# Optimization experiments

Hardware: AMD Instinct MI355X
Metric: run time of the kernel (lower is better)

## Reference

```python
import jax, jax.numpy as jnp
import numpy as np

N_NODES = 4096
N_EDGES = 32768
PE_DIM = 16
HIDDEN = 128


def setup_inputs() -> dict:
    key = jax.random.key(0)
    k_nodes, k_send, k_recv, k_w = jax.random.split(key, 4)
    nodes = jax.random.normal(k_nodes, (N_NODES, 8), dtype=jnp.float32)
    senders = jax.random.randint(k_send, (N_EDGES,), 0, N_NODES)
    receivers = jax.random.randint(k_recv, (N_EDGES,), 0, N_NODES)
    W = jax.random.normal(k_w, (PE_DIM, HIDDEN), dtype=jnp.float32) / np.sqrt(PE_DIM).astype(np.float32)
    b = jnp.zeros((HIDDEN,), dtype=jnp.float32)
    return {"nodes": nodes, "senders": senders, "receivers": receivers, "W": W, "b": b}


def reference(nodes, senders, receivers, W, b):
    n = nodes.shape[0]
    pe_dim = W.shape[0]
    # out-degree per node (clamped at 1, as in the original)
    ones = jnp.ones(senders.shape[0], dtype=jnp.float32)
    degree = jnp.maximum(jax.ops.segment_sum(ones, senders, num_segments=n), 1.0)
    inv_deg_e = (1.0 / degree)[senders]  # [E], per-edge 1/deg(sender)

    prob = jnp.eye(n, dtype=jnp.float32)  # [n, n] landing probabilities
    diags = []
    for _ in range(pe_dim):
        # gather sender rows, normalize, scatter-add into receiver rows
        msg = prob[senders] * inv_deg_e[:, None]           # [E, n]
        prob = jax.ops.segment_sum(msg, receivers, num_segments=n)  # [n, n]
        diags.append(jnp.diagonal(prob))                    # return probability A^k_ii
    pe = jnp.stack(diags, axis=-1)  # [n, pe_dim]
    return pe @ W + b               # [n, hidden]
```

## Files before the change

### kernel.cpp

```cpp
#include <hip/hip_runtime.h>

#define NN 4096
#define NE 32768
#define PED 16
#define HID 128
#define CW 16
#define NCHUNK 64
#define THREADS 1024
#define PASSES 4

typedef _Float16 h_t;
typedef _Float16 h8 __attribute__((ext_vector_type(8)));
typedef unsigned long long u64;

__device__ __forceinline__ int xp(int p) {
  int g = ((p & 3) << 1) | ((p >> 2) & 1);
  return ((p >> 2) << 7) | (g << 4);
}


__global__ void count_kernel(const int* __restrict__ senders,
                             const int* __restrict__ receivers,
                             int* __restrict__ outdeg, int* __restrict__ indeg) {
  int e = blockIdx.x * blockDim.x + threadIdx.x;
  if (e < NE) {
    atomicAdd(&outdeg[senders[e]], 1);
    atomicAdd(&indeg[receivers[e]], 1);
  }
}

__global__ void perm_kernel(const int* __restrict__ outdeg, int* __restrict__ indeg,
                            float* __restrict__ dinv, int* __restrict__ fillc,
                            int* __restrict__ rowperm, int* __restrict__ sortpos,
                            int* __restrict__ chunk_off, int* __restrict__ chunk_len) {
  __shared__ int ld_d[NN];
  __shared__ int hist[64];
  __shared__ int hbase[64];
  int t = threadIdx.x;
  if (t < 64) hist[t] = 0;
  __syncthreads();
  for (int r = t; r < NN; r += 1024) {
    int od = outdeg[r]; if (od < 1) od = 1;
    dinv[r] = 1.0f / (float)od;
    fillc[r] = 0;
    int d = indeg[r]; if (d > 63) d = 63;
    ld_d[r] = d;
    indeg[r] = d;
    atomicAdd(&hist[d], 1);
  }
  __syncthreads();
  if (t == 0) {
    int acc = 0;
    for (int i = 0; i < 64; ++i) { hbase[i] = acc; acc += hist[i]; }
  }
  __syncthreads();
  for (int r = t; r < NN; r += 1024) {
    int pos = atomicAdd(&hbase[ld_d[r]], 1);
    rowperm[pos] = r;
    sortpos[r] = pos;
  }
  __syncthreads();
  if (t < NCHUNK) {
    int m = 0;
    for (int i = 0; i < 64; ++i) {
      int d = ld_d[rowperm[(t << 6) + i]];
      if (d > m) m = d;
    }
    chunk_len[t] = (m + 1) & ~1;
  }
  __syncthreads();
  if (t == 0) {
    int acc = 0;
    for (int c = 0; c < NCHUNK; ++c) { chunk_off[c] = acc; acc += chunk_len[c] << 6; }
    chunk_off[NCHUNK] = acc;
  }
}

__global__ void fill_ell(const int* __restrict__ senders, const int* __restrict__ receivers,
                         const int* __restrict__ sortpos, const int* __restrict__ chunk_off,
                         const float* __restrict__ dinv, int* __restrict__ fillc,
                         int2* __restrict__ ell) {
  int e = blockIdx.x * blockDim.x + threadIdx.x;
  if (e < NE) {
    int r = receivers[e], s = senders[e];
    int p = sortpos[r];
    int tslot = atomicAdd(&fillc[r], 1);
    int slot = chunk_off[p >> 6] + (tslot << 6) + (p & 63);
    ell[slot] = make_int2(xp(sortpos[s]), __float_as_int(dinv[s]));
  }
}

__global__ void sched_ell(const int* __restrict__ chunk_off,
                          const int* __restrict__ chunk_len,
                          const int* __restrict__ rowperm,
                          const int* __restrict__ indeg,
                          const int2* __restrict__ src, int2* __restrict__ dst) {
  int tid = blockIdx.x * blockDim.x + threadIdx.x;
  if (tid >= NCHUNK * 8) return;
  {
    int total = chunk_off[NCHUNK];
    for (int i = tid; i < 2048; i += 512) dst[total + i] = make_int2(0, 0);
  }
  int c = tid >> 3;
  int trk = tid & 7;
  int base = chunk_off[c];
  int len = chunk_len[c];
  int l0 = trk << 3;

  int d[8];
  u64 freeL[8];
  int dmax = 0;
#pragma unroll
  for (int j = 0; j < 8; ++j) {
    int dd = indeg[rowperm[(c << 6) + l0 + j]];
    d[j] = dd;
    if (dd > dmax) dmax = dd;
  }
  if (len > 63) {
#pragma unroll
    for (int j = 0; j < 8; ++j) {
      for (int t = 0; t < d[j]; ++t) dst[base + (t << 6) + l0 + j] = src[base + (t << 6) + l0 + j];
      for (int t = d[j]; t < len; ++t) dst[base + (t << 6) + l0 + j] = make_int2(((t + j) & 7) << 4, 0);
    }
    return;
  }
  u64 full = (len == 0) ? 0 : ((1ull << len) - 1);
#pragma unroll
  for (int j = 0; j < 8; ++j) freeL[j] = full;
  u64 fC[8];
#pragma unroll
  for (int q = 0; q < 8; ++q) fC[q] = full;

  int2 cur[8], nxt[8];
#pragma unroll
  for (int j = 0; j < 8; ++j) cur[j] = src[base + l0 + j];
  for (int t = 0; t < dmax; ++t) {
#pragma unroll
    for (int j = 0; j < 8; ++j) nxt[j] = src[base + ((t + 1) << 6) + l0 + j];
#pragma unroll
    for (int j = 0; j < 8; ++j) {
      if (t < d[j]) {
        int2 e = cur[j];
        int cls = (e.x >> 4) & 7;
        u64 fc = 0;
#pragma unroll
        for (int q = 0; q < 8; ++q) fc = (q == cls) ? fC[q] : fc;
        u64 avail = freeL[j] & fc;
        u64 pool = avail ? avail : freeL[j];
        u64 pick = pool & (~pool + 1);
        int slab = __builtin_ctzll(pick);
        freeL[j] &= ~pick;
        if (avail) {
#pragma unroll
          for (int q = 0; q < 8; ++q) if (q == cls) fC[q] &= ~pick;
        }
        dst[base + (slab << 6) + l0 + j] = e;
      }
    }
#pragma unroll
    for (int j = 0; j < 8; ++j) cur[j] = nxt[j];
  }
#pragma unroll
  for (int j = 0; j < 8; ++j) {
    u64 rem = freeL[j];
    while (rem) {
      u64 pick = rem & (~rem + 1);
      rem &= rem - 1;
      int slab = __builtin_ctzll(pick);
      int cls = 0;
#pragma unroll
      for (int q = 7; q >= 0; --q) if (fC[q] & pick) cls = q;
#pragma unroll
      for (int q = 0; q < 8; ++q) if (q == cls) fC[q] &= ~pick;
      dst[base + (slab << 6) + l0 + j] = make_int2(cls << 4, 0);
    }
  }
}


#define MIXL(acc, srcv) \
  asm("v_fma_mix_f32 %0, %1, %2, %0 op_sel_hi:[1,0,0]" : "+v"(acc) : "v"(srcv), "v"(w))
#define MIXH(acc, srcv) \
  asm("v_fma_mix_f32 %0, %1, %2, %0 op_sel:[1,0,0] op_sel_hi:[1,0,0]" : "+v"(acc) : "v"(srcv), "v"(w))

#define MIX16(lo, hi) \
  MIXL(a[0], lo.x);  MIXH(a[1], lo.x);  \
  MIXL(a[2], lo.y);  MIXH(a[3], lo.y);  \
  MIXL(a[4], lo.z);  MIXH(a[5], lo.z);  \
  MIXL(a[6], lo.w);  MIXH(a[7], lo.w);  \
  MIXL(a[8], hi.x);  MIXH(a[9], hi.x);  \
  MIXL(a[10], hi.y); MIXH(a[11], hi.y); \
  MIXL(a[12], hi.z); MIXH(a[13], hi.z); \
  MIXL(a[14], hi.w); MIXH(a[15], hi.w)

__global__ __launch_bounds__(THREADS, 4)
void fused_kernel(const int2* __restrict__ ell,
                  const int* __restrict__ chunk_off,
                  const int* __restrict__ chunk_len,
                  const int* __restrict__ rowperm,
                  const float* __restrict__ W,
                  const float* __restrict__ bvec,
                  float* __restrict__ out) {
  __shared__ __align__(16) h_t X[NN * CW];
  __shared__ float pe_lds[CW * PED];
  char* Xb = (char*)X;
  int c0 = blockIdx.x * CW;
  int tid = threadIdx.x;
  int wave = tid >> 6, lane = tid & 63;

  int baseB[PASSES], lenB[PASSES], djB[PASSES], xbW[PASSES];
#pragma unroll
  for (int pass = 0; pass < PASSES; ++pass) {
    int chunk = (pass << 4) + ((pass & 1) ? (15 - wave) : wave);
    baseB[pass] = chunk_off[chunk];
    lenB[pass] = chunk_len[chunk];
    djB[pass] = rowperm[(chunk << 6) + lane] - c0;
    xbW[pass] = xp((chunk << 6) + lane);
  }

  for (int p = tid; p < NN; p += THREADS) {
    int dd = rowperm[p] - c0;
    h8 lo8, hi8;
#pragma unroll
    for (int j = 0; j < 8; ++j) {
      lo8[j] = (h_t)((dd == j) ? 1.0f : 0.0f);
      hi8[j] = (h_t)((dd == 8 + j) ? 1.0f : 0.0f);
    }
    int xb = xp(p);
    *reinterpret_cast<h8*>(Xb + xb) = lo8;
    *reinterpret_cast<h8*>(Xb + (xb ^ 16)) = hi8;
  }
  __syncthreads();

  for (int k = 0; k < PED; ++k) {
    h8 rlo[PASSES], rhi[PASSES];
#pragma unroll
    for (int pass = 0; pass < PASSES; ++pass) {
      int base = baseB[pass];
      int len = lenB[pass];
      float a[16];
#pragma unroll
      for (int j = 0; j < 16; ++j) a[j] = 0.f;
      const int2* ep = ell + base + lane;
      int2 e0 = ep[0];
      int2 e1 = ep[64];
      int2 e2 = ep[128];
      int2 e3 = ep[192];
      int4 lo0 = *reinterpret_cast<const int4*>(Xb + e0.x);
      int4 hi0 = *reinterpret_cast<const int4*>(Xb + (e0.x ^ 16));
      for (int t = 0; t < len; t += 2) {
        int2 e4 = ep[256], e5 = ep[320];
        ep += 128;
        int4 lo1 = *reinterpret_cast<const int4*>(Xb + e1.x);
        int4 hi1 = *reinterpret_cast<const int4*>(Xb + (e1.x ^ 16));
        float w = __int_as_float(e0.y);
        MIX16(lo0, hi0);
        int4 nlo = *reinterpret_cast<const int4*>(Xb + e2.x);
        int4 nhi = *reinterpret_cast<const int4*>(Xb + (e2.x ^ 16));
        w = __int_as_float(e1.y);
        MIX16(lo1, hi1);
        e0 = e2; e1 = e3; e2 = e4; e3 = e5;
        lo0 = nlo; hi0 = nhi;
      }
      h8 plo, phi;
#pragma unroll
      for (int j = 0; j < 8; ++j) { plo[j] = (h_t)a[j]; phi[j] = (h_t)a[8 + j]; }
      rlo[pass] = plo; rhi[pass] = phi;
      int dj = djB[pass];
      if (dj >= 0 && dj < CW) {
        float dv = a[0];
#pragma unroll
        for (int j = 1; j < 16; ++j) dv = (dj == j) ? a[j] : dv;
        pe_lds[dj * PED + k] = dv;
      }
    }
    if (k != PED - 1) {
      __syncthreads();
#pragma unroll
      for (int pass = 0; pass < PASSES; ++pass) {
        int xb = xbW[pass];
        *reinterpret_cast<h8*>(Xb + xb) = rlo[pass];
        *reinterpret_cast<h8*>(Xb + (xb ^ 16)) = rhi[pass];
      }
      __syncthreads();
    }
  }
  __syncthreads();

  {
    int h = tid & 127;
    int r0 = tid >> 7;
    float wcol[PED];
#pragma unroll
    for (int kk = 0; kk < PED; ++kk) wcol[kk] = W[kk * HID + h];
    float bb = bvec[h];
#pragma unroll
    for (int half = 0; half < 2; ++half) {
      int row = r0 + (half << 3);
      float acc = bb;
#pragma unroll
      for (int kk = 0; kk < PED; ++kk) acc = fmaf(pe_lds[row * PED + kk], wcol[kk], acc);
      out[(size_t)(c0 + row) * HID + h] = acc;
    }
  }
}

extern "C" void kernel_launch(void* const* d_in, const int* in_sizes, int n_in,
                              void* d_out, int out_size, void* d_ws, size_t ws_size,
                              hipStream_t stream) {
  const int* senders = (const int*)d_in[1];
  const int* receivers = (const int*)d_in[2];
  const float* W = (const float*)d_in[3];
  const float* bvec = (const float*)d_in[4];
  float* out = (float*)d_out;

  char* p = (char*)d_ws;
  int* outdeg = (int*)p;    p += (size_t)NN * 4;
  int* indeg = (int*)p;     p += (size_t)NN * 4;
  int* fillc = (int*)p;     p += (size_t)NN * 4;
  float* dinv = (float*)p;  p += (size_t)NN * 4;
  int* rowperm = (int*)p;   p += (size_t)NN * 4;
  int* sortpos = (int*)p;   p += (size_t)NN * 4;
  int* chunk_off = (int*)p; p += 128 * 4;
  int* chunk_len = (int*)p; p += 128 * 4;
  size_t ell_slots = (size_t)64 * NE + 2048;
  int2* ell = (int2*)p;     p += ell_slots * sizeof(int2);
  int2* ell2 = (int2*)p;

  hipMemsetAsync(d_ws, 0, (size_t)NN * 4 * 2, stream);
  count_kernel<<<NE / 256, 256, 0, stream>>>(senders, receivers, outdeg, indeg);
  perm_kernel<<<1, 1024, 0, stream>>>(outdeg, indeg, dinv, fillc,
                                      rowperm, sortpos, chunk_off, chunk_len);
  fill_ell<<<NE / 256, 256, 0, stream>>>(senders, receivers, sortpos, chunk_off, dinv, fillc, ell);
  sched_ell<<<8, 64, 0, stream>>>(chunk_off, chunk_len, rowperm, indeg, ell, ell2);

  fused_kernel<<<NN / CW, THREADS, 0, stream>>>(ell2, chunk_off, chunk_len, rowperm, W, bvec, out);
}
```

Before: 206.7 us.

## Fuse graph preprocessing kernels into a single-block prep kernel using shared memory

Merges the memset, degree count, permutation, ELL fill and scheduling kernels into one 1024-thread single-block kernel. Degrees, sort positions, inverse degrees and fill counters now live in shared memory instead of global workspace. This removes several launches and global round trips. In exchange, the edge counting and ELL fill that used to run across many blocks now run on one block, and the scheduling step drops its software prefetch of the next slab.

```diff
diff --git a/kernel.cpp b/kernel.cpp
--- a/kernel.cpp
+++ b/kernel.cpp
@@ -18,161 +18,141 @@
   return ((p >> 2) << 7) | (g << 4);
 }
 
-
-__global__ void count_kernel(const int* __restrict__ senders,
-                             const int* __restrict__ receivers,
-                             int* __restrict__ outdeg, int* __restrict__ indeg) {
-  int e = blockIdx.x * blockDim.x + threadIdx.x;
-  if (e < NE) {
-    atomicAdd(&outdeg[senders[e]], 1);
-    atomicAdd(&indeg[receivers[e]], 1);
-  }
-}
-
-__global__ void perm_kernel(const int* __restrict__ outdeg, int* __restrict__ indeg,
-                            float* __restrict__ dinv, int* __restrict__ fillc,
-                            int* __restrict__ rowperm, int* __restrict__ sortpos,
-                            int* __restrict__ chunk_off, int* __restrict__ chunk_len) {
+__global__ __launch_bounds__(1024)
+void prep_all(const int* __restrict__ senders, const int* __restrict__ receivers,
+              int* __restrict__ rowperm_g, int* __restrict__ chunk_off_g,
+              int* __restrict__ chunk_len_g,
+              int2* __restrict__ esrc, int2* __restrict__ edst) {
+  __shared__ int ld_out[NN];
   __shared__ int ld_d[NN];
+  __shared__ int sortpos_l[NN];
+  __shared__ int rowperm_l[NN];
+  __shared__ float dinv_l[NN];
+  __shared__ int fillc_l[NN];
   __shared__ int hist[64];
   __shared__ int hbase[64];
+  __shared__ int coff[NCHUNK + 1];
+  __shared__ int clen[NCHUNK];
   int t = threadIdx.x;
+
+  for (int i = t; i < NN; i += 1024) { ld_out[i] = 0; ld_d[i] = 0; fillc_l[i] = 0; }
   if (t < 64) hist[t] = 0;
   __syncthreads();
+  for (int e = t; e < NE; e += 1024) {
+    atomicAdd(&ld_out[senders[e]], 1);
+    atomicAdd(&ld_d[receivers[e]], 1);
+  }
+  __syncthreads();
   for (int r = t; r < NN; r += 1024) {
-    int od = outdeg[r]; if (od < 1) od = 1;
-    dinv[r] = 1.0f / (float)od;
-    fillc[r] = 0;
-    int d = indeg[r]; if (d > 63) d = 63;
+    int od = ld_out[r]; if (od < 1) od = 1;
+    dinv_l[r] = 1.0f / (float)od;
+    int d = ld_d[r]; if (d > 63) d = 63;
     ld_d[r] = d;
-    indeg[r] = d;
     atomicAdd(&hist[d], 1);
+  }
+  __syncthreads();
+  if (t == 0) { int acc = 0; for (int i = 0; i < 64; ++i) { hbase[i] = acc; acc += hist[i]; } }
+  __syncthreads();
+  for (int r = t; r < NN; r += 1024) {
+    int pos = atomicAdd(&hbase[ld_d[r]], 1);
+    rowperm_l[pos] = r;
+    sortpos_l[r] = pos;
+  }
+  __syncthreads();
+  if (t < NCHUNK) {
+    int m = 0;
+    for (int i = 0; i < 64; ++i) { int d = ld_d[rowperm_l[(t << 6) + i]]; if (d > m) m = d; }
+    clen[t] = (m + 1) & ~1;
   }
   __syncthreads();
   if (t == 0) {
     int acc = 0;
-    for (int i = 0; i < 64; ++i) { hbase[i] = acc; acc += hist[i]; }
-  }
-  __syncthreads();
-  for (int r = t; r < NN; r += 1024) {
-    int pos = atomicAdd(&hbase[ld_d[r]], 1);
-    rowperm[pos] = r;
-    sortpos[r] = pos;
-  }
-  __syncthreads();
-  if (t < NCHUNK) {
-    int m = 0;
-    for (int i = 0; i < 64; ++i) {
-      int d = ld_d[rowperm[(t << 6) + i]];
-      if (d > m) m = d;
-    }
-    chunk_len[t] = (m + 1) & ~1;
-  }
-  __syncthreads();
-  if (t == 0) {
-    int acc = 0;
-    for (int c = 0; c < NCHUNK; ++c) { chunk_off[c] = acc; acc += chunk_len[c] << 6; }
-    chunk_off[NCHUNK] = acc;
-  }
-}
-
-__global__ void fill_ell(const int* __restrict__ senders, const int* __restrict__ receivers,
-                         const int* __restrict__ sortpos, const int* __restrict__ chunk_off,
-                         const float* __restrict__ dinv, int* __restrict__ fillc,
-                         int2* __restrict__ ell) {
-  int e = blockIdx.x * blockDim.x + threadIdx.x;
-  if (e < NE) {
+    for (int c = 0; c < NCHUNK; ++c) { coff[c] = acc; acc += clen[c] << 6; }
+    coff[NCHUNK] = acc;
+  }
+  __syncthreads();
+  for (int i = t; i < NN; i += 1024) rowperm_g[i] = rowperm_l[i];
+  if (t < NCHUNK) chunk_len_g[t] = clen[t];
+  if (t <= NCHUNK) chunk_off_g[t] = coff[t];
+  for (int e = t; e < NE; e += 1024) {
     int r = receivers[e], s = senders[e];
-    int p = sortpos[r];
-    int tslot = atomicAdd(&fillc[r], 1);
-    int slot = chunk_off[p >> 6] + (tslot << 6) + (p & 63);
-    ell[slot] = make_int2(xp(sortpos[s]), __float_as_int(dinv[s]));
-  }
-}
-
-__global__ void sched_ell(const int* __restrict__ chunk_off,
-                          const int* __restrict__ chunk_len,
-                          const int* __restrict__ rowperm,
-                          const int* __restrict__ indeg,
-                          const int2* __restrict__ src, int2* __restrict__ dst) {
-  int tid = blockIdx.x * blockDim.x + threadIdx.x;
-  if (tid >= NCHUNK * 8) return;
-  {
-    int total = chunk_off[NCHUNK];
-    for (int i = tid; i < 2048; i += 512) dst[total + i] = make_int2(0, 0);
-  }
-  int c = tid >> 3;
-  int trk = tid & 7;
-  int base = chunk_off[c];
-  int len = chunk_len[c];
-  int l0 = trk << 3;
-
-  int d[8];
-  u64 freeL[8];
-  int dmax = 0;
-#pragma unroll
-  for (int j = 0; j < 8; ++j) {
-    int dd = indeg[rowperm[(c << 6) + l0 + j]];
-    d[j] = dd;
-    if (dd > dmax) dmax = dd;
-  }
-  if (len > 63) {
+    int p = sortpos_l[r];
+    int tslot = atomicAdd(&fillc_l[r], 1);
+    int slot = coff[p >> 6] + (tslot << 6) + (p & 63);
+    esrc[slot] = make_int2(xp(sortpos_l[s]), __float_as_int(dinv_l[s]));
+  }
+  __threadfence();
+  __syncthreads();
+  int total = coff[NCHUNK];
+  for (int i = t; i < 2048; i += 1024) edst[total + i] = make_int2(0, 0);
+  if (t < NCHUNK * 8) {
+    int c = t >> 3;
+    int trk = t & 7;
+    int base = coff[c];
+    int len = clen[c];
+    int l0 = trk << 3;
+    int d[8];
+    u64 freeL[8];
+    int dmax = 0;
 #pragma unroll
     for (int j = 0; j < 8; ++j) {
-      for (int t = 0; t < d[j]; ++t) dst[base + (t << 6) + l0 + j] = src[base + (t << 6) + l0 + j];
-      for (int t = d[j]; t < len; ++t) dst[base + (t << 6) + l0 + j] = make_int2(((t + j) & 7) << 4, 0);
-    }
-    return;
-  }
-  u64 full = (len == 0) ? 0 : ((1ull << len) - 1);
-#pragma unroll
-  for (int j = 0; j < 8; ++j) freeL[j] = full;
-  u64 fC[8];
-#pragma unroll
-  for (int q = 0; q < 8; ++q) fC[q] = full;
-
-  int2 cur[8], nxt[8];
-#pragma unroll
-  for (int j = 0; j < 8; ++j) cur[j] = src[base + l0 + j];
-  for (int t = 0; t < dmax; ++t) {
-#pragma unroll
-    for (int j = 0; j < 8; ++j) nxt[j] = src[base + ((t + 1) << 6) + l0 + j];
+      int dd = ld_d[rowperm_l[(c << 6) + l0 + j]];
+      d[j] = dd;
+      if (dd > dmax) dmax = dd;
+    }
+    if (len > 63) {
+#pragma unroll
+      for (int j = 0; j < 8; ++j) {
+        for (int tt = 0; tt < d[j]; ++tt) edst[base + (tt << 6) + l0 + j] = esrc[base + (tt << 6) + l0 + j];
+        for (int tt = d[j]; tt < len; ++tt) edst[base + (tt << 6) + l0 + j] = make_int2(((tt + j) & 7) << 4, 0);
+      }
+      return;
+    }
+    u64 full = (len == 0) ? 0 : ((1ull << len) - 1);
+#pragma unroll
+    for (int j = 0; j < 8; ++j) freeL[j] = full;
+    u64 fC[8];
+#pragma unroll
+    for (int q = 0; q < 8; ++q) fC[q] = full;
+    for (int tt = 0; tt < dmax; ++tt) {
+      int2 cur[8];
+#pragma unroll
+      for (int j = 0; j < 8; ++j) cur[j] = esrc[base + (tt << 6) + l0 + j];
+#pragma unroll
+      for (int j = 0; j < 8; ++j) {
+        if (tt < d[j]) {
+          int2 e = cur[j];
+          int cls = (e.x >> 4) & 7;
+          u64 fc = 0;
+#pragma unroll
+          for (int q = 0; q < 8; ++q) fc = (q == cls) ? fC[q] : fc;
+          u64 avail = freeL[j] & fc;
+          u64 pool = avail ? avail : freeL[j];
+          u64 pick = pool & (~pool + 1);
+          int slab = __builtin_ctzll(pick);
+          freeL[j] &= ~pick;
+          if (avail) {
+#pragma unroll
+            for (int q = 0; q < 8; ++q) if (q == cls) fC[q] &= ~pick;
+          }
+          edst[base + (slab << 6) + l0 + j] = e;
+        }
+      }
+    }
 #pragma unroll
     for (int j = 0; j < 8; ++j) {
-      if (t < d[j]) {
-        int2 e = cur[j];
-        int cls = (e.x >> 4) & 7;
-        u64 fc = 0;
-#pragma unroll
-        for (int q = 0; q < 8; ++q) fc = (q == cls) ? fC[q] : fc;
-        u64 avail = freeL[j] & fc;
-        u64 pool = avail ? avail : freeL[j];
-        u64 pick = pool & (~pool + 1);
+      u64 rem = freeL[j];
+      while (rem) {
+        u64 pick = rem & (~rem + 1);
+        rem &= rem - 1;
         int slab = __builtin_ctzll(pick);
-        freeL[j] &= ~pick;
-        if (avail) {
-#pragma unroll
-          for (int q = 0; q < 8; ++q) if (q == cls) fC[q] &= ~pick;
-        }
-        dst[base + (slab << 6) + l0 + j] = e;
-      }
-    }
-#pragma unroll
-    for (int j = 0; j < 8; ++j) cur[j] = nxt[j];
-  }
-#pragma unroll
-  for (int j = 0; j < 8; ++j) {
-    u64 rem = freeL[j];
-    while (rem) {
-      u64 pick = rem & (~rem + 1);
-      rem &= rem - 1;
-      int slab = __builtin_ctzll(pick);
-      int cls = 0;
-#pragma unroll
-      for (int q = 7; q >= 0; --q) if (fC[q] & pick) cls = q;
-#pragma unroll
-      for (int q = 0; q < 8; ++q) if (q == cls) fC[q] &= ~pick;
-      dst[base + (slab << 6) + l0 + j] = make_int2(cls << 4, 0);
+        int cls = 0;
+#pragma unroll
+        for (int q = 7; q >= 0; --q) if (fC[q] & pick) cls = q;
+#pragma unroll
+        for (int q = 0; q < 8; ++q) if (q == cls) fC[q] &= ~pick;
+        edst[base + (slab << 6) + l0 + j] = make_int2(cls << 4, 0);
+      }
     }
   }
 }
@@ -315,24 +295,13 @@
   float* out = (float*)d_out;
 
   char* p = (char*)d_ws;
-  int* outdeg = (int*)p;    p += (size_t)NN * 4;
-  int* indeg = (int*)p;     p += (size_t)NN * 4;
-  int* fillc = (int*)p;     p += (size_t)NN * 4;
-  float* dinv = (float*)p;  p += (size_t)NN * 4;
   int* rowperm = (int*)p;   p += (size_t)NN * 4;
-  int* sortpos = (int*)p;   p += (size_t)NN * 4;
   int* chunk_off = (int*)p; p += 128 * 4;
   int* chunk_len = (int*)p; p += 128 * 4;
   size_t ell_slots = (size_t)64 * NE + 2048;
   int2* ell = (int2*)p;     p += ell_slots * sizeof(int2);
   int2* ell2 = (int2*)p;
 
-  hipMemsetAsync(d_ws, 0, (size_t)NN * 4 * 2, stream);
-  count_kernel<<<NE / 256, 256, 0, stream>>>(senders, receivers, outdeg, indeg);
-  perm_kernel<<<1, 1024, 0, stream>>>(outdeg, indeg, dinv, fillc,
-                                      rowperm, sortpos, chunk_off, chunk_len);
-  fill_ell<<<NE / 256, 256, 0, stream>>>(senders, receivers, sortpos, chunk_off, dinv, fillc, ell);
-  sched_ell<<<8, 64, 0, stream>>>(chunk_off, chunk_len, rowperm, indeg, ell, ell2);
-
+  prep_all<<<1, 1024, 0, stream>>>(senders, receivers, rowperm, chunk_off, chunk_len, ell, ell2);
   fused_kernel<<<NN / CW, THREADS, 0, stream>>>(ell2, chunk_off, chunk_len, rowperm, W, bvec, out);
 }
```

After: 239.3 us. 15.8% more time.

## Merge preprocessing kernels into one cooperative kernel with grid syncs

Applied to the files above, without the earlier changes.

Replaces the memset plus four small preprocessing launches (degree count, permutation, ELL fill, ELL scheduling) with a single cooperative kernel that separates the phases with grid.sync. The goal is to remove per-launch overhead and inter-kernel gaps ahead of the main fused kernel. The trade-off is the cost of grid-wide barriers, and the permutation phase now runs on a single 512-thread block. It also clamps the fill slot to under 64 and handles len>=64 in the scheduler bitmask.

```diff
diff --git a/kernel.cpp b/kernel.cpp
--- a/kernel.cpp
+++ b/kernel.cpp
@@ -1,4 +1,7 @@
 #include <hip/hip_runtime.h>
+#include <hip/hip_cooperative_groups.h>
+
+namespace cg = cooperative_groups;
 
 #define NN 4096
 #define NE 32768
@@ -18,161 +21,144 @@
   return ((p >> 2) << 7) | (g << 4);
 }
 
-
-__global__ void count_kernel(const int* __restrict__ senders,
-                             const int* __restrict__ receivers,
-                             int* __restrict__ outdeg, int* __restrict__ indeg) {
-  int e = blockIdx.x * blockDim.x + threadIdx.x;
-  if (e < NE) {
-    atomicAdd(&outdeg[senders[e]], 1);
-    atomicAdd(&indeg[receivers[e]], 1);
-  }
-}
-
-__global__ void perm_kernel(const int* __restrict__ outdeg, int* __restrict__ indeg,
-                            float* __restrict__ dinv, int* __restrict__ fillc,
-                            int* __restrict__ rowperm, int* __restrict__ sortpos,
-                            int* __restrict__ chunk_off, int* __restrict__ chunk_len) {
+__global__ __launch_bounds__(512)
+void prep_coop(const int* __restrict__ senders, const int* __restrict__ receivers,
+               float* __restrict__ dinv, int* __restrict__ sortpos,
+               int* __restrict__ rowperm, int* __restrict__ indeg,
+               int* __restrict__ outdeg, int* __restrict__ fillc,
+               int* __restrict__ chunk_off, int* __restrict__ chunk_len,
+               int2* __restrict__ esrc, int2* __restrict__ edst) {
+  cg::grid_group grid = cg::this_grid();
   __shared__ int ld_d[NN];
-  __shared__ int hist[64];
-  __shared__ int hbase[64];
-  int t = threadIdx.x;
-  if (t < 64) hist[t] = 0;
-  __syncthreads();
-  for (int r = t; r < NN; r += 1024) {
-    int od = outdeg[r]; if (od < 1) od = 1;
-    dinv[r] = 1.0f / (float)od;
-    fillc[r] = 0;
-    int d = indeg[r]; if (d > 63) d = 63;
-    ld_d[r] = d;
-    indeg[r] = d;
-    atomicAdd(&hist[d], 1);
-  }
-  __syncthreads();
-  if (t == 0) {
-    int acc = 0;
-    for (int i = 0; i < 64; ++i) { hbase[i] = acc; acc += hist[i]; }
-  }
-  __syncthreads();
-  for (int r = t; r < NN; r += 1024) {
-    int pos = atomicAdd(&hbase[ld_d[r]], 1);
-    rowperm[pos] = r;
-    sortpos[r] = pos;
-  }
-  __syncthreads();
-  if (t < NCHUNK) {
-    int m = 0;
-    for (int i = 0; i < 64; ++i) {
-      int d = ld_d[rowperm[(t << 6) + i]];
-      if (d > m) m = d;
-    }
-    chunk_len[t] = (m + 1) & ~1;
-  }
-  __syncthreads();
-  if (t == 0) {
-    int acc = 0;
-    for (int c = 0; c < NCHUNK; ++c) { chunk_off[c] = acc; acc += chunk_len[c] << 6; }
-    chunk_off[NCHUNK] = acc;
-  }
-}
-
-__global__ void fill_ell(const int* __restrict__ senders, const int* __restrict__ receivers,
-                         const int* __restrict__ sortpos, const int* __restrict__ chunk_off,
-                         const float* __restrict__ dinv, int* __restrict__ fillc,
-                         int2* __restrict__ ell) {
-  int e = blockIdx.x * blockDim.x + threadIdx.x;
-  if (e < NE) {
-    int r = receivers[e], s = senders[e];
+  __shared__ int rp[NN];
+  __shared__ int hist[64], hbase[64];
+  int tid = blockIdx.x * 512 + threadIdx.x;
+
+  if (tid < NN) { outdeg[tid] = 0; indeg[tid] = 0; fillc[tid] = 0; }
+  grid.sync();
+
+  atomicAdd(&outdeg[senders[tid]], 1);
+  atomicAdd(&indeg[receivers[tid]], 1);
+  grid.sync();
+
+  if (blockIdx.x == 0) {
+    int t = threadIdx.x;
+    if (t < 64) hist[t] = 0;
+    __syncthreads();
+    for (int r = t; r < NN; r += 512) {
+      int od = outdeg[r]; if (od < 1) od = 1;
+      dinv[r] = 1.0f / (float)od;
+      int d = indeg[r]; if (d > 63) d = 63;
+      ld_d[r] = d;
+      indeg[r] = d;
+      atomicAdd(&hist[d], 1);
+    }
+    __syncthreads();
+    if (t == 0) { int acc = 0; for (int i = 0; i < 64; ++i) { hbase[i] = acc; acc += hist[i]; } }
+    __syncthreads();
+    for (int r = t; r < NN; r += 512) {
+      int pos = atomicAdd(&hbase[ld_d[r]], 1);
+      rp[pos] = r;
+      sortpos[r] = pos;
+    }
+    __syncthreads();
+    for (int i = t; i < NN; i += 512) rowperm[i] = rp[i];
+    if (t < NCHUNK) {
+      int m = 0;
+      for (int i = 0; i < 64; ++i) { int d = ld_d[rp[(t << 6) + i]]; if (d > m) m = d; }
+      chunk_len[t] = (m + 1) & ~1;
+    }
+    __syncthreads();
+    if (t == 0) {
+      int acc = 0;
+      for (int c = 0; c < NCHUNK; ++c) { chunk_off[c] = acc; acc += chunk_len[c] << 6; }
+      chunk_off[NCHUNK] = acc;
+    }
+  }
+  __threadfence();
+  grid.sync();
+
+  {
+    int r = receivers[tid], s = senders[tid];
     int p = sortpos[r];
-    int tslot = atomicAdd(&fillc[r], 1);
-    int slot = chunk_off[p >> 6] + (tslot << 6) + (p & 63);
-    ell[slot] = make_int2(xp(sortpos[s]), __float_as_int(dinv[s]));
-  }
-}
-
-__global__ void sched_ell(const int* __restrict__ chunk_off,
-                          const int* __restrict__ chunk_len,
-                          const int* __restrict__ rowperm,
-                          const int* __restrict__ indeg,
-                          const int2* __restrict__ src, int2* __restrict__ dst) {
-  int tid = blockIdx.x * blockDim.x + threadIdx.x;
-  if (tid >= NCHUNK * 8) return;
+    int ts = atomicAdd(&fillc[r], 1);
+    if (ts < 64) {
+      int slot = chunk_off[p >> 6] + (ts << 6) + (p & 63);
+      esrc[slot] = make_int2(xp(sortpos[s]), __float_as_int(dinv[s]));
+    }
+  }
+  __threadfence();
+  grid.sync();
+
   {
     int total = chunk_off[NCHUNK];
-    for (int i = tid; i < 2048; i += 512) dst[total + i] = make_int2(0, 0);
-  }
-  int c = tid >> 3;
-  int trk = tid & 7;
-  int base = chunk_off[c];
-  int len = chunk_len[c];
-  int l0 = trk << 3;
-
-  int d[8];
-  u64 freeL[8];
-  int dmax = 0;
-#pragma unroll
-  for (int j = 0; j < 8; ++j) {
-    int dd = indeg[rowperm[(c << 6) + l0 + j]];
-    d[j] = dd;
-    if (dd > dmax) dmax = dd;
-  }
-  if (len > 63) {
+    if (tid >= 512 && tid < 512 + 2048) edst[total + (tid - 512)] = make_int2(0, 0);
+  }
+  if (tid < NCHUNK * 8) {
+    int c = tid >> 3;
+    int trk = tid & 7;
+    int base = chunk_off[c];
+    int len = chunk_len[c];
+    int l0 = trk << 3;
+    int d[8];
+    u64 freeL[8];
+    int dmax = 0;
 #pragma unroll
     for (int j = 0; j < 8; ++j) {
-      for (int t = 0; t < d[j]; ++t) dst[base + (t << 6) + l0 + j] = src[base + (t << 6) + l0 + j];
-      for (int t = d[j]; t < len; ++t) dst[base + (t << 6) + l0 + j] = make_int2(((t + j) & 7) << 4, 0);
-    }
-    return;
-  }
-  u64 full = (len == 0) ? 0 : ((1ull << len) - 1);
-#pragma unroll
-  for (int j = 0; j < 8; ++j) freeL[j] = full;
-  u64 fC[8];
-#pragma unroll
-  for (int q = 0; q < 8; ++q) fC[q] = full;
-
-  int2 cur[8], nxt[8];
-#pragma unroll
-  for (int j = 0; j < 8; ++j) cur[j] = src[base + l0 + j];
-  for (int t = 0; t < dmax; ++t) {
-#pragma unroll
-    for (int j = 0; j < 8; ++j) nxt[j] = src[base + ((t + 1) << 6) + l0 + j];
+      int dd = indeg[rowperm[(c << 6) + l0 + j]];
+      d[j] = dd;
+      if (dd > dmax) dmax = dd;
+    }
+    u64 full = (len >= 64) ? ~0ull : ((len == 0) ? 0 : ((1ull << len) - 1));
+#pragma unroll
+    for (int j = 0; j < 8; ++j) freeL[j] = full;
+    u64 fC[8];
+#pragma unroll
+    for (int q = 0; q < 8; ++q) fC[q] = full;
+
+    int2 cur[8], nxt[8];
+#pragma unroll
+    for (int j = 0; j < 8; ++j) cur[j] = esrc[base + l0 + j];
+    for (int tt = 0; tt < dmax; ++tt) {
+#pragma unroll
+      for (int j = 0; j < 8; ++j) nxt[j] = esrc[base + ((tt + 1) << 6) + l0 + j];
+#pragma unroll
+      for (int j = 0; j < 8; ++j) {
+        if (tt < d[j]) {
+          int2 e = cur[j];
+          int cls = (e.x >> 4) & 7;
+          u64 fc = 0;
+#pragma unroll
+          for (int q = 0; q < 8; ++q) fc = (q == cls) ? fC[q] : fc;
+          u64 avail = freeL[j] & fc;
+          u64 pool = avail ? avail : freeL[j];
+          u64 pick = pool & (~pool + 1);
+          int slab = __builtin_ctzll(pick);
+          freeL[j] &= ~pick;
+          if (avail) {
+#pragma unroll
+            for (int q = 0; q < 8; ++q) if (q == cls) fC[q] &= ~pick;
+          }
+          edst[base + (slab << 6) + l0 + j] = e;
+        }
+      }
+#pragma unroll
+      for (int j = 0; j < 8; ++j) cur[j] = nxt[j];
+    }
 #pragma unroll
     for (int j = 0; j < 8; ++j) {
-      if (t < d[j]) {
-        int2 e = cur[j];
-        int cls = (e.x >> 4) & 7;
-        u64 fc = 0;
-#pragma unroll
-        for (int q = 0; q < 8; ++q) fc = (q == cls) ? fC[q] : fc;
-        u64 avail = freeL[j] & fc;
-        u64 pool = avail ? avail : freeL[j];
-        u64 pick = pool & (~pool + 1);
+      u64 rem = freeL[j];
+      while (rem) {
+        u64 pick = rem & (~rem + 1);
+        rem &= rem - 1;
         int slab = __builtin_ctzll(pick);
-        freeL[j] &= ~pick;
-        if (avail) {
-#pragma unroll
-          for (int q = 0; q < 8; ++q) if (q == cls) fC[q] &= ~pick;
-        }
-        dst[base + (slab << 6) + l0 + j] = e;
-      }
-    }
-#pragma unroll
-    for (int j = 0; j < 8; ++j) cur[j] = nxt[j];
-  }
-#pragma unroll
-  for (int j = 0; j < 8; ++j) {
-    u64 rem = freeL[j];
-    while (rem) {
-      u64 pick = rem & (~rem + 1);
-      rem &= rem - 1;
-      int slab = __builtin_ctzll(pick);
-      int cls = 0;
-#pragma unroll
-      for (int q = 7; q >= 0; --q) if (fC[q] & pick) cls = q;
-#pragma unroll
-      for (int q = 0; q < 8; ++q) if (q == cls) fC[q] &= ~pick;
-      dst[base + (slab << 6) + l0 + j] = make_int2(cls << 4, 0);
+        int cls = 0;
+#pragma unroll
+        for (int q = 7; q >= 0; --q) if (fC[q] & pick) cls = q;
+#pragma unroll
+        for (int q = 0; q < 8; ++q) if (q == cls) fC[q] &= ~pick;
+        edst[base + (slab << 6) + l0 + j] = make_int2(cls << 4, 0);
+      }
     }
   }
 }
@@ -319,20 +305,20 @@
   int* indeg = (int*)p;     p += (size_t)NN * 4;
   int* fillc = (int*)p;     p += (size_t)NN * 4;
   float* dinv = (float*)p;  p += (size_t)NN * 4;
+  int* sortpos = (int*)p;   p += (size_t)NN * 4;
   int* rowperm = (int*)p;   p += (size_t)NN * 4;
-  int* sortpos = (int*)p;   p += (size_t)NN * 4;
   int* chunk_off = (int*)p; p += 128 * 4;
   int* chunk_len = (int*)p; p += 128 * 4;
-  size_t ell_slots = (size_t)64 * NE + 2048;
-  int2* ell = (int2*)p;     p += ell_slots * sizeof(int2);
-  int2* ell2 = (int2*)p;
-
-  hipMemsetAsync(d_ws, 0, (size_t)NN * 4 * 2, stream);
-  count_kernel<<<NE / 256, 256, 0, stream>>>(senders, receivers, outdeg, indeg);
-  perm_kernel<<<1, 1024, 0, stream>>>(outdeg, indeg, dinv, fillc,
-                                      rowperm, sortpos, chunk_off, chunk_len);
-  fill_ell<<<NE / 256, 256, 0, stream>>>(senders, receivers, sortpos, chunk_off, dinv, fillc, ell);
-  sched_ell<<<8, 64, 0, stream>>>(chunk_off, chunk_len, rowperm, indeg, ell, ell2);
-
-  fused_kernel<<<NN / CW, THREADS, 0, stream>>>(ell2, chunk_off, chunk_len, rowperm, W, bvec, out);
+  size_t ell_slots = (size_t)NCHUNK * 64 * 64 + 2048;
+  int2* esrc = (int2*)p;    p += ell_slots * sizeof(int2);
+  int2* edst = (int2*)p;
+
+  void* args[] = {
+    (void*)&senders, (void*)&receivers, (void*)&dinv, (void*)&sortpos,
+    (void*)&rowperm, (void*)&indeg, (void*)&outdeg, (void*)&fillc,
+    (void*)&chunk_off, (void*)&chunk_len, (void*)&esrc, (void*)&edst
+  };
+  hipLaunchCooperativeKernel((void*)prep_coop, dim3(NE / 512), dim3(512), args, 0, stream);
+
+  fused_kernel<<<NN / CW, THREADS, 0, stream>>>(edst, chunk_off, chunk_len, rowperm, W, bvec, out);
 }
```

New measurement: 286.6 us. +38.7%, slower.
